# Kernel tuning notes

Measured on AMD Instinct MI355X. Metric: run time of the kernel, lower is better.

The kernel has to match this reference:

```python
import jax, jax.numpy as jnp
import numpy as np

T = 2048        # Tmax encoder frames
EPROJS = 1024   # encoder projection dim (Henc)
DUNITS = 512    # prediction net hidden
EMBED = 512     # embedding dim
JOINT = 512     # joint space dim
ODIM = 10000    # output vocab
BLANK = 0


def setup_inputs() -> dict:
    key = jax.random.key(0)
    ks = jax.random.split(key, 11)
    def g(k, shape, scale):
        return (jax.random.normal(k, shape, dtype=jnp.float32) * scale)
    inp = {
        'h': jax.random.normal(ks[0], (T, EPROJS), dtype=jnp.float32),
        # Embedding with padding_idx=blank -> blank row zeroed
        'embed': g(ks[1], (ODIM, EMBED), 0.05).at[BLANK].set(0.0),
        # LSTMCell params (torch gate order: i, f, g, o)
        'W_ih': g(ks[2], (4 * DUNITS, EMBED), 1.0 / np.sqrt(EMBED)),
        'W_hh': g(ks[3], (4 * DUNITS, DUNITS), 1.0 / np.sqrt(DUNITS)),
        'b_ih': g(ks[4], (4 * DUNITS,), 0.01),
        'b_hh': g(ks[5], (4 * DUNITS,), 0.01),
        # joint network
        'W_enc': g(ks[6], (JOINT, EPROJS), 1.0 / np.sqrt(EPROJS)),
        'b_enc': g(ks[7], (JOINT,), 0.01),
        'W_dec': g(ks[8], (JOINT, DUNITS), 1.0 / np.sqrt(DUNITS)),  # no bias
        'W_out': g(ks[9], (ODIM, JOINT), 1.0 / np.sqrt(JOINT)),
        'b_out': g(ks[10], (ODIM,), 0.01),
    }
    return inp


def _lstm_cell(x, h_prev, c_prev, W_ih, W_hh, b_ih, b_hh):
    gates = W_ih @ x + b_ih + W_hh @ h_prev + b_hh  # (4*DUNITS,)
    i, f, g, o = jnp.split(gates, 4)
    c = jax.nn.sigmoid(f) * c_prev + jax.nn.sigmoid(i) * jnp.tanh(g)
    h = jax.nn.sigmoid(o) * jnp.tanh(c)
    return h, c


def reference(h, embed, W_ih, W_hh, b_ih, b_hh, W_enc, b_enc, W_dec, W_out, b_out):
    # Precompute encoder-side joint projection (same math, hoisted out of loop)
    h_proj = h @ W_enc.T + b_enc  # (T, JOINT)

    # Initial prediction-net step on zero embedding from zero state
    zeros_e = jnp.zeros((EMBED,), dtype=h.dtype)
    zeros_d = jnp.zeros((DUNITS,), dtype=h.dtype)
    y0, c0 = _lstm_cell(zeros_e, zeros_d, zeros_d, W_ih, W_hh, b_ih, b_hh)

    def step(carry, hp_t):
        y, c, score = carry
        # joint: tanh(lin_enc(h_t) + lin_dec(y)) -> lin_out -> log_softmax
        ytu = jax.nn.log_softmax(W_out @ jnp.tanh(hp_t + W_dec @ y) + b_out)
        logp = jnp.max(ytu)
        pred = jnp.argmax(ytu)
        emitted = pred != BLANK
        # Candidate prediction-net update with embedded token
        ey = embed[pred]
        y_new, c_new = _lstm_cell(ey, y, c, W_ih, W_hh, b_ih, b_hh)
        y = jnp.where(emitted, y_new, y)
        c = jnp.where(emitted, c_new, c)
        score = score + jnp.where(emitted, logp, jnp.zeros_like(logp))
        tok = jnp.where(emitted, pred, BLANK).astype(jnp.int32)
        return (y, c, score), tok

    (y, c, score), yseq = jax.lax.scan(step, (y0, c0, jnp.float32(0.0)), h_proj)
    # yseq: (T,) int32, BLANK where no symbol was emitted at that frame
    return yseq, score
```

## Files before the change

### kernel.cpp

```cpp
#include <hip/hip_runtime.h>
#include <stdint.h>

typedef unsigned long long u64;
typedef uint32_t u32;

#define NB     256
#define NT     256
#define TMAX   2048
#define EPROJS 1024
#define DUNITS 512
#define EMBED  512
#define JOINT  512
#define ODIM   10000

#define N_LSTM 32
#define CONS0  32
#define N_CONS 223
#define AGG_B  255
#define MAGIC  0xD07ED07Eu

#define WS_PK   0
#define WS_SA   7168
#define WS_DN   14336
#define WS_AGG  15360
#define WS_Y    16384
#define WS_U    20480
#define WS_PART 24576
#define WS_HP   155648

__device__ __forceinline__ float aloadf(const float* p){
  return __hip_atomic_load(p, __ATOMIC_RELAXED, __HIP_MEMORY_SCOPE_AGENT);
}
__device__ __forceinline__ void astoref(float* p, float v){
  __hip_atomic_store(p, v, __ATOMIC_RELAXED, __HIP_MEMORY_SCOPE_AGENT);
}
__device__ __forceinline__ u64 aloadu64(const u64* p){
  return __hip_atomic_load(p, __ATOMIC_RELAXED, __HIP_MEMORY_SCOPE_AGENT);
}
__device__ __forceinline__ void astoreu64(u64* p, u64 v){
  __hip_atomic_store(p, v, __ATOMIC_RELAXED, __HIP_MEMORY_SCOPE_AGENT);
}
__device__ __forceinline__ u32 aloadu32(const u32* p){
  return __hip_atomic_load(p, __ATOMIC_RELAXED, __HIP_MEMORY_SCOPE_AGENT);
}
__device__ __forceinline__ void astoreu32(u32* p, u32 v){
  __hip_atomic_store(p, v, __ATOMIC_RELAXED, __HIP_MEMORY_SCOPE_AGENT);
}

__device__ __forceinline__ u32 ordbits(float f){
  u32 u = __float_as_uint(f);
  return (u & 0x80000000u) ? ~u : (u | 0x80000000u);
}
__device__ __forceinline__ float unordbits(u32 o){
  u32 u = (o & 0x80000000u) ? (o & 0x7fffffffu) : ~o;
  return __uint_as_float(u);
}
__device__ __forceinline__ float sigmoidf_(float x){ return 1.0f/(1.0f+expf(-x)); }

__device__ __forceinline__ float wredsum(float v){
  #pragma unroll
  for (int o=32;o>0;o>>=1) v += __shfl_xor(v, o);
  return v;
}
__device__ __forceinline__ u64 wredmax64(u64 v){
  #pragma unroll
  for (int o=32;o>0;o>>=1){ u64 x = __shfl_xor(v, o); v = (x>v)?x:v; }
  return v;
}

__device__ __forceinline__ int zslot(int j){
  return (j&7)*64 + ((j>>3) ^ ((j&7)<<2));
}

#define LOAD8(dst, baseptr) { const float4* _p=(const float4*)(baseptr); \
  float4 _a=_p[0], _b=_p[1]; \
  dst[0]=_a.x; dst[1]=_a.y; dst[2]=_a.z; dst[3]=_a.w; \
  dst[4]=_b.x; dst[5]=_b.y; dst[6]=_b.z; dst[7]=_b.w; }

__global__ void rnnt_init(char* ws){
  u32* p = (u32*)ws;
  const int stride = blockDim.x * gridDim.x;
  for (int i = blockIdx.x*blockDim.x + threadIdx.x; i < 38912; i += stride) p[i] = 0u;
}

__global__ void __launch_bounds__(NT, 1)
rnnt_decode(const float* __restrict__ h,    const float* __restrict__ embed,
            const float* __restrict__ W_ih, const float* __restrict__ W_hh,
            const float* __restrict__ b_ih, const float* __restrict__ b_hh,
            const float* __restrict__ W_enc,const float* __restrict__ b_enc,
            const float* __restrict__ W_dec,const float* __restrict__ W_out,
            const float* __restrict__ b_out,
            float* __restrict__ out, char* __restrict__ ws)
{
  const int b    = blockIdx.x;
  const int tid  = threadIdx.x;
  const int lane = tid & 63;
  const int w    = tid >> 6;

  u64*  ytag  = (u64*)(ws + WS_Y);
  u64*  utag  = (u64*)(ws + WS_U);
  u64*  ptag  = (u64*)(ws + WS_PART);
  u64*  pkall = (u64*)(ws + WS_PK);
  u64*  saall = (u64*)(ws + WS_SA);
  u32*  done  = (u32*)(ws + WS_DN);
  u32*  aggr  = (u32*)(ws + WS_AGG);
  float* hp   = (float*)(ws + WS_HP);

  __shared__ float smem[8192];
  float* PL = smem;
  float* GL = &smem[4416];
  u64*   R64= (u64*)&smem[4480];
  float* RF = &smem[4488];
  float* YO = &smem[4492];
  float* ZL = &smem[4544];
  float* PS = &smem[5056];

  {
    float (*lds_h)[EPROJS] = (float(*)[EPROJS])smem;
    #pragma unroll
    for (int r=0;r<8;r++){
      const float4 hv = *(const float4*)(h + (size_t)(8*b + r)*EPROJS + tid*4);
      *(float4*)&lds_h[r][tid*4] = hv;
    }
    __syncthreads();
    for (int p=0;p<2;p++){
      const int j = p*NT + tid;
      float acc[8] = {0,0,0,0,0,0,0,0};
      const float4* wrow = (const float4*)(W_enc + (size_t)j*EPROJS);
      for (int k4=0;k4<EPROJS/4;k4++){
        const float4 wv = wrow[k4];
        #pragma unroll
        for (int t8=0;t8<8;t8++){
          const float4 hv = *(const float4*)&lds_h[t8][k4*4];
          acc[t8] = fmaf(wv.x,hv.x, fmaf(wv.y,hv.y, fmaf(wv.z,hv.z, fmaf(wv.w,hv.w, acc[t8]))));
        }
      }
      const float be = b_enc[j];
      #pragma unroll
      for (int t8=0;t8<8;t8++)
        astoref(&hp[(size_t)(8*b+t8)*JOINT + j], acc[t8] + be);
    }
    asm volatile("s_waitcnt vmcnt(0)" ::: "memory");
    if (tid==0) astoreu32(&done[b], MAGIC);
    __syncthreads();
  }

  if (b < N_LSTM){
    const int d = b;
    float wih[16][8], whh[16][8];
    #pragma unroll
    for (int q=0;q<16;q++){
      const int gr = w*DUNITS + 16*d + q;
      LOAD8(wih[q], W_ih + (size_t)gr*EMBED  + lane*8);
      LOAD8(whh[q], W_hh + (size_t)gr*DUNITS + lane*8);
    }
    float wdc0[16], wdc1[16];
    {
      const float4* p0 = (const float4*)(W_dec + (size_t)(2*tid)*DUNITS   + 16*d);
      const float4* p1 = (const float4*)(W_dec + (size_t)(2*tid+1)*DUNITS + 16*d);
      #pragma unroll
      for (int k4=0;k4<4;k4++){
        const float4 a = p0[k4];
        wdc0[4*k4+0]=a.x; wdc0[4*k4+1]=a.y; wdc0[4*k4+2]=a.z; wdc0[4*k4+3]=a.w;
        const float4 c = p1[k4];
        wdc1[4*k4+0]=c.x; wdc1[4*k4+1]=c.y; wdc1[4*k4+2]=c.z; wdc1[4*k4+3]=c.w;
      }
    }
    float bias_r = 0.0f;
    if (tid < 64){
      const int gr = (tid>>4)*DUNITS + 16*d + (tid&15);
      bias_r = b_ih[gr] + b_hh[gr];
    }
    float c_st = 0.0f, y_st = 0.0f;
    if (tid < 16){
      const int j = 16*d + tid;
      const float gi = b_ih[j]            + b_hh[j];
      const float gg = b_ih[2*DUNITS + j] + b_hh[2*DUNITS + j];
      const float go = b_ih[3*DUNITS + j] + b_hh[3*DUNITS + j];
      c_st = sigmoidf_(gi)*tanhf(gg);
      y_st = sigmoidf_(go)*tanhf(c_st);
      YO[tid] = y_st;
      astoreu64(&ytag[j], ((u64)1u<<32) | (u64)__float_as_uint(y_st));
    }
    __syncthreads();
    {
      float p0=0.f, p1=0.f;
      #pragma unroll
      for (int k=0;k<16;k++){ p0 = fmaf(wdc0[k], YO[k], p0); p1 = fmaf(wdc1[k], YO[k], p1); }
      u64* up = ptag + (size_t)d*512;
      astoreu64(&up[2*tid],   ((u64)1u<<32) | (u64)__float_as_uint(p0));
      astoreu64(&up[2*tid+1], ((u64)1u<<32) | (u64)__float_as_uint(p1));
    }

    const int jj = tid & 15;
    const int pp = tid >> 4;
    for (int t=0;t<TMAX;t++){
      const u32 g = (u32)(t+1);
      u64 pv0, pv1, yv[8];
      for(;;){
        pv0 = aloadu64(&ptag[(size_t)(2*pp)*512   + 16*d + jj]);
        pv1 = aloadu64(&ptag[(size_t)(2*pp+1)*512 + 16*d + jj]);
        bool ok = ((u32)(pv0>>32)==g) & ((u32)(pv1>>32)==g);
        #pragma unroll
        for (int i=0;i<8;i++){
          yv[i] = aloadu64(&ytag[8*lane + i]);
          ok &= ((u32)(yv[i]>>32) == g);
        }
        if (ok) break;
        __builtin_amdgcn_s_sleep(1);
      }
      float y8[8];
      #pragma unroll
      for (int i=0;i<8;i++) y8[i] = __uint_as_float((u32)yv[i]);
      PS[jj*17 + pp] = __uint_as_float((u32)pv0) + __uint_as_float((u32)pv1);
      __syncthreads();
      if (tid < 16){
        float s = 0.f;
        #pragma unroll
        for (int k=0;k<16;k++) s += PS[tid*17 + k];
        astoreu64(&utag[16*d + tid], ((u64)g<<32) | (u64)__float_as_uint(s));
      }
      float vp[16];
      #pragma unroll
      for (int q=0;q<16;q++){
        float a=0.f;
        #pragma unroll
        for (int k=0;k<8;k++) a = fmaf(whh[q][k], y8[k], a);
        vp[q] = a;
      }
      u64 pk = 0;
      {
        const u64* pks = pkall + (g&3)*224;
        for(;;){
          pk = (tid < N_CONS) ? aloadu64(&pks[tid]) : 0;
          const int ok = (tid < N_CONS) ? ((u32)(pk>>48) >= g) : 1;
          if (__all(ok)) break;
          __builtin_amdgcn_s_sleep(1);
        }
      }
      const u64 m = wredmax64(pk);
      if (lane==0) R64[w] = m;
      const int predw = (int)((~(u32)m) & 0xFFFFu);
      float e8[8];
      LOAD8(e8, embed + (size_t)predw*EMBED + 8*lane);
      __syncthreads();
      u64 best = R64[0];
      #pragma unroll
      for (int i=1;i<4;i++){ const u64 x=R64[i]; best = (x>best)?x:best; }
      const int pred = (int)((~(u32)best) & 0xFFFFu);
      const int emitted = (pred != 0);
      if (m != best){
        LOAD8(e8, embed + (size_t)pred*EMBED + 8*lane);
      }
      #pragma unroll
      for (int q=0;q<16;q++){
        float a = vp[q];
        #pragma unroll
        for (int k=0;k<8;k++) a = fmaf(wih[q][k], e8[k], a);
        PL[(w*16+q)*68 + lane] = a;
      }
      __syncthreads();
      if (tid < 64){
        const float* row = &PL[tid*68];
        float s = bias_r;
        #pragma unroll
        for (int k4=0;k4<16;k4++){
          const float4 v4 = *(const float4*)&row[4*k4];
          s += v4.x + v4.y + v4.z + v4.w;
        }
        GL[tid] = s;
      }
      __syncthreads();
      if (tid < 16){
        const float gi=GL[tid], gf=GL[16+tid], gg=GL[32+tid], go=GL[48+tid];
        const float cn = sigmoidf_(gf)*c_st + sigmoidf_(gi)*tanhf(gg);
        const float yn = sigmoidf_(go)*tanhf(cn);
        if (emitted){ c_st = cn; y_st = yn; }
        YO[tid] = y_st;
        if (t < TMAX-1)
          astoreu64(&ytag[16*d + tid], ((u64)(g+1)<<32) | (u64)__float_as_uint(y_st));
      }
      __syncthreads();
      if (t < TMAX-1){
        float p0=0.f, p1=0.f;
        #pragma unroll
        for (int k=0;k<16;k++){ p0 = fmaf(wdc0[k], YO[k], p0); p1 = fmaf(wdc1[k], YO[k], p1); }
        u64* up = ptag + (size_t)d*512;
        astoreu64(&up[2*tid],   ((u64)(g+1)<<32) | (u64)__float_as_uint(p0));
        astoreu64(&up[2*tid+1], ((u64)(g+1)<<32) | (u64)__float_as_uint(p1));
      }
    }
  }
  else if (b < AGG_B){
    const int cb = b - CONS0;
    int rowstart, rowcnt;
    if (cb < 188){ rowstart = cb*45;                 rowcnt = 45; }
    else         { rowstart = 8460 + (cb-188)*44;    rowcnt = 44; }
    float wout[12][8];
    #pragma unroll
    for (int q=0;q<12;q++){
      const int s = 12*w + q;
      if (s < rowcnt){
        LOAD8(wout[q], W_out + (size_t)(rowstart+s)*JOINT + lane*8);
      } else {
        #pragma unroll
        for (int k=0;k<8;k++) wout[q][k]=0.f;
      }
    }
    float my_bo = 0.f; int my_row = 0; bool my_val = false;
    if (tid < rowcnt){ my_val = true; my_row = rowstart + tid; my_bo = b_out[my_row]; }
    const u32* agrep = &aggr[(cb&7)*32];

    for(;;){
      const u32 dv = aloadu32(&done[tid]);
      if (__all(dv == MAGIC)) break;
      __builtin_amdgcn_s_sleep(2);
    }
    __syncthreads();

    const int j0 = 2*tid, j1 = 2*tid+1;
    const int s0 = zslot(j0), s1 = zslot(j1);
    for (int t=0;t<TMAX;t++){
      const u32 g = (u32)(t+1);
      const float2 h2 = *(const float2*)(hp + (size_t)t*JOINT + j0);
      u64 ua, ub2;
      for(;;){
        ua  = aloadu64(&utag[j0]);
        ub2 = aloadu64(&utag[j1]);
        if ( (((u32)(ua>>32))==g) & (((u32)(ub2>>32))==g) ) break;
        __builtin_amdgcn_s_sleep(1);
      }
      ZL[s0] = tanhf(h2.x + __uint_as_float((u32)ua));
      ZL[s1] = tanhf(h2.y + __uint_as_float((u32)ub2));
      __syncthreads();
      float z8[8];
      #pragma unroll
      for (int e=0;e<8;e++) z8[e] = ZL[e*64 + (lane ^ (e<<2))];
      #pragma unroll
      for (int q=0;q<12;q++){
        float a=0.f;
        #pragma unroll
        for (int k=0;k<8;k++) a = fmaf(wout[q][k], z8[k], a);
        PL[(12*w+q)*68 + lane] = a;
      }
      __syncthreads();
      u64 key = 0; float lg = 0.f;
      if (tid < 48){
        const float* row = &PL[tid*68];
        float s = my_bo;
        #pragma unroll
        for (int k4=0;k4<16;k4++){
          const float4 v4 = *(const float4*)&row[4*k4];
          s += v4.x + v4.y + v4.z + v4.w;
        }
        lg = s;
        if (my_val) key = ((u64)ordbits(lg)<<16) | (u64)(0xFFFFu & ~(u32)my_row);
      }
      if (w == 0){
        const u64 bk = wredmax64(key);
        const float mw = unordbits((u32)(bk>>16));
        const float e  = my_val ? __expf(lg - mw) : 0.f;
        const float sw = wredsum(e);
        if (lane == 0){
          while ((int)(g - aloadu32(agrep)) > 3) __builtin_amdgcn_s_sleep(2);
          astoreu64(&saall[(g&3)*224 + cb], ((u64)g<<32) | (u64)__float_as_uint(sw));
          astoreu64(&pkall[(g&3)*224 + cb], ((u64)g<<48) | bk);
        }
      }
    }
  }
  else {
    float score = 0.0f;
    for (int t=0;t<TMAX;t++){
      const u32 g = (u32)(t+1);
      const u64* pks = pkall + (g&3)*224;
      const u64* sas = saall + (g&3)*224;
      u64 pk=0, sa=0;
      for(;;){
        if (tid < N_CONS){ pk = aloadu64(&pks[tid]); sa = aloadu64(&sas[tid]); }
        const int ok = (tid < N_CONS) ? (((u32)(pk>>48)==g) & (((u32)(sa>>32))==g)) : 1;
        if (__all(ok)) break;
        __builtin_amdgcn_s_sleep(2);
      }
      { u64 m = wredmax64(pk); if (lane==0) R64[w]=m; }
      __syncthreads();
      u64 best = R64[0];
      #pragma unroll
      for (int i=1;i<4;i++){ const u64 x=R64[i]; best = (x>best)?x:best; }
      const float mstar = unordbits((u32)(best>>16));
      float term = (tid < N_CONS) ?
        __uint_as_float((u32)sa) * __expf(unordbits((u32)(pk>>16)) - mstar) : 0.f;
      term = wredsum(term);
      if (lane==0) RF[w] = term;
      __syncthreads();
      if (tid==0){
        const float S = RF[0]+RF[1]+RF[2]+RF[3];
        const int pred = (int)((~(u32)best) & 0xFFFFu);
        if (pred != 0) score += -logf(S);
        out[t] = (float)pred;
      }
      __syncthreads();
      if (tid < 8) astoreu32(&aggr[tid*32], g);
    }
    if (tid==0) out[TMAX] = score;
  }
}

extern "C" void kernel_launch(void* const* d_in, const int* in_sizes, int n_in,
                              void* d_out, int out_size, void* d_ws, size_t ws_size,
                              hipStream_t stream)
{
  const float* h     = (const float*)d_in[0];
  const float* embed = (const float*)d_in[1];
  const float* W_ih  = (const float*)d_in[2];
  const float* W_hh  = (const float*)d_in[3];
  const float* b_ih  = (const float*)d_in[4];
  const float* b_hh  = (const float*)d_in[5];
  const float* W_enc = (const float*)d_in[6];
  const float* b_enc = (const float*)d_in[7];
  const float* W_dec = (const float*)d_in[8];
  const float* W_out = (const float*)d_in[9];
  const float* b_out = (const float*)d_in[10];
  float* out = (float*)d_out;
  char* ws = (char*)d_ws;

  hipLaunchKernelGGL(rnnt_init, dim3(32), dim3(NT), 0, stream, ws);
  hipLaunchKernelGGL(rnnt_decode, dim3(NB), dim3(NT), 0, stream,
                     h, embed, W_ih, W_hh, b_ih, b_hh, W_enc, b_enc, W_dec, W_out, b_out,
                     out, ws);
}
```

Before: 17.70 ms.

## Replace tagged partial-sum exchange with atomicAdd reduction and counter barrier

LSTM blocks now accumulate their W_dec partial products straight into a double-buffered, 8-way replicated float buffer with atomicAdd and bump per-replica counters. Consumer blocks spin on a single counter and sum the 8 replicas themselves. This removes the second-level tagged reduction stage in the LSTM blocks and the per-element tag polling, and swaps wave-level __all spins with sleeps for block-wide __syncthreads_and polling. The cost is float atomics (non-deterministic summation order), explicit zeroing of buffers each step, and extra block barriers.

```diff
diff --git a/kernel.cpp b/kernel.cpp
--- a/kernel.cpp
+++ b/kernel.cpp
@@ -23,10 +23,10 @@
 #define WS_SA   7168
 #define WS_DN   14336
 #define WS_AGG  15360
-#define WS_Y    16384
-#define WS_U    20480
-#define WS_PART 24576
-#define WS_HP   155648
+#define WS_CNT  16384
+#define WS_Y    17408
+#define WS_U    21504
+#define WS_HP   54272
 
 __device__ __forceinline__ float aloadf(const float* p){
   return __hip_atomic_load(p, __ATOMIC_RELAXED, __HIP_MEMORY_SCOPE_AGENT);
@@ -80,7 +80,7 @@
 __global__ void rnnt_init(char* ws){
   u32* p = (u32*)ws;
   const int stride = blockDim.x * gridDim.x;
-  for (int i = blockIdx.x*blockDim.x + threadIdx.x; i < 38912; i += stride) p[i] = 0u;
+  for (int i = blockIdx.x*blockDim.x + threadIdx.x; i < 13568; i += stride) p[i] = 0u;
 }
 
 __global__ void __launch_bounds__(NT, 1)
@@ -97,13 +97,13 @@
   const int lane = tid & 63;
   const int w    = tid >> 6;
 
-  u64*  ytag  = (u64*)(ws + WS_Y);
-  u64*  utag  = (u64*)(ws + WS_U);
-  u64*  ptag  = (u64*)(ws + WS_PART);
+  u64*   ytag = (u64*)(ws + WS_Y);
+  float* ubuf = (float*)(ws + WS_U);
   u64*  pkall = (u64*)(ws + WS_PK);
   u64*  saall = (u64*)(ws + WS_SA);
   u32*  done  = (u32*)(ws + WS_DN);
   u32*  aggr  = (u32*)(ws + WS_AGG);
+  u32*  cnt   = (u32*)(ws + WS_CNT);
   float* hp   = (float*)(ws + WS_HP);
 
   __shared__ float smem[8192];
@@ -112,8 +112,7 @@
   u64*   R64= (u64*)&smem[4480];
   float* RF = &smem[4488];
   float* YO = &smem[4492];
-  float* ZL = &smem[4544];
-  float* PS = &smem[5056];
+  float* SL = &smem[4544];
 
   {
     float (*lds_h)[EPROJS] = (float(*)[EPROJS])smem;
@@ -187,39 +186,28 @@
       float p0=0.f, p1=0.f;
       #pragma unroll
       for (int k=0;k<16;k++){ p0 = fmaf(wdc0[k], YO[k], p0); p1 = fmaf(wdc1[k], YO[k], p1); }
-      u64* up = ptag + (size_t)d*512;
-      astoreu64(&up[2*tid],   ((u64)1u<<32) | (u64)__float_as_uint(p0));
-      astoreu64(&up[2*tid+1], ((u64)1u<<32) | (u64)__float_as_uint(p1));
-    }
-
-    const int jj = tid & 15;
-    const int pp = tid >> 4;
+      float* up = ubuf + 1*4096 + (d&7)*512;
+      atomicAdd(&up[2*tid],   p0);
+      atomicAdd(&up[2*tid+1], p1);
+    }
+    asm volatile("s_waitcnt vmcnt(0)" ::: "memory");
+    __syncthreads();
+    if (tid < 8) atomicAdd(&cnt[tid*32], 1u);
+
     for (int t=0;t<TMAX;t++){
       const u32 g = (u32)(t+1);
-      u64 pv0, pv1, yv[8];
+      u64 ya, yb;
       for(;;){
-        pv0 = aloadu64(&ptag[(size_t)(2*pp)*512   + 16*d + jj]);
-        pv1 = aloadu64(&ptag[(size_t)(2*pp+1)*512 + 16*d + jj]);
-        bool ok = ((u32)(pv0>>32)==g) & ((u32)(pv1>>32)==g);
-        #pragma unroll
-        for (int i=0;i<8;i++){
-          yv[i] = aloadu64(&ytag[8*lane + i]);
-          ok &= ((u32)(yv[i]>>32) == g);
-        }
-        if (ok) break;
-        __builtin_amdgcn_s_sleep(1);
-      }
+        ya = aloadu64(&ytag[2*tid]); yb = aloadu64(&ytag[2*tid+1]);
+        const int ok = ((u32)(ya>>32)==g) & ((u32)(yb>>32)==g);
+        if (__syncthreads_and(ok)) break;
+      }
+      SL[zslot(2*tid)]   = __uint_as_float((u32)ya);
+      SL[zslot(2*tid+1)] = __uint_as_float((u32)yb);
+      __syncthreads();
       float y8[8];
       #pragma unroll
-      for (int i=0;i<8;i++) y8[i] = __uint_as_float((u32)yv[i]);
-      PS[jj*17 + pp] = __uint_as_float((u32)pv0) + __uint_as_float((u32)pv1);
-      __syncthreads();
-      if (tid < 16){
-        float s = 0.f;
-        #pragma unroll
-        for (int k=0;k<16;k++) s += PS[tid*17 + k];
-        astoreu64(&utag[16*d + tid], ((u64)g<<32) | (u64)__float_as_uint(s));
-      }
+      for (int e=0;e<8;e++) y8[e] = SL[e*64 + (lane ^ (e<<2))];
       float vp[16];
       #pragma unroll
       for (int q=0;q<16;q++){
@@ -229,14 +217,10 @@
         vp[q] = a;
       }
       u64 pk = 0;
-      {
-        const u64* pks = pkall + (g&3)*224;
-        for(;;){
-          pk = (tid < N_CONS) ? aloadu64(&pks[tid]) : 0;
-          const int ok = (tid < N_CONS) ? ((u32)(pk>>48) >= g) : 1;
-          if (__all(ok)) break;
-          __builtin_amdgcn_s_sleep(1);
-        }
+      for(;;){
+        if (tid < N_CONS) pk = aloadu64(&pkall[(g&3)*224 + tid]);
+        const int ok = (tid < N_CONS) ? ((u32)(pk>>48) >= g) : 1;
+        if (__syncthreads_and(ok)) break;
       }
       const u64 m = wredmax64(pk);
       if (lane==0) R64[w] = m;
@@ -251,6 +235,10 @@
       const int emitted = (pred != 0);
       if (m != best){
         LOAD8(e8, embed + (size_t)pred*EMBED + 8*lane);
+      }
+      if (tid < 64){
+        u64* uz = (u64*)(ubuf + (g&1)*4096 + (d&7)*512) + (d>>3)*64;
+        astoreu64(&uz[tid], 0ull);
       }
       #pragma unroll
       for (int q=0;q<16;q++){
@@ -285,10 +273,13 @@
         float p0=0.f, p1=0.f;
         #pragma unroll
         for (int k=0;k<16;k++){ p0 = fmaf(wdc0[k], YO[k], p0); p1 = fmaf(wdc1[k], YO[k], p1); }
-        u64* up = ptag + (size_t)d*512;
-        astoreu64(&up[2*tid],   ((u64)(g+1)<<32) | (u64)__float_as_uint(p0));
-        astoreu64(&up[2*tid+1], ((u64)(g+1)<<32) | (u64)__float_as_uint(p1));
-      }
+        float* up = ubuf + ((g+1)&1)*4096 + (d&7)*512;
+        atomicAdd(&up[2*tid],   p0);
+        atomicAdd(&up[2*tid+1], p1);
+      }
+      asm volatile("s_waitcnt vmcnt(0)" ::: "memory");
+      __syncthreads();
+      if (t < TMAX-1 && tid < 8) atomicAdd(&cnt[tid*32], 1u);
     }
   }
   else if (b < AGG_B){
@@ -312,30 +303,36 @@
     const u32* agrep = &aggr[(cb&7)*32];
 
     for(;;){
-      const u32 dv = aloadu32(&done[tid]);
-      if (__all(dv == MAGIC)) break;
-      __builtin_amdgcn_s_sleep(2);
-    }
-    __syncthreads();
-
+      const int ok = (aloadu32(&done[tid]) == MAGIC);
+      if (__syncthreads_and(ok)) break;
+    }
+
+    const u32* cp = &cnt[(cb&7)*32];
     const int j0 = 2*tid, j1 = 2*tid+1;
     const int s0 = zslot(j0), s1 = zslot(j1);
     for (int t=0;t<TMAX;t++){
       const u32 g = (u32)(t+1);
       const float2 h2 = *(const float2*)(hp + (size_t)t*JOINT + j0);
-      u64 ua, ub2;
-      for(;;){
-        ua  = aloadu64(&utag[j0]);
-        ub2 = aloadu64(&utag[j1]);
-        if ( (((u32)(ua>>32))==g) & (((u32)(ub2>>32))==g) ) break;
-        __builtin_amdgcn_s_sleep(1);
-      }
-      ZL[s0] = tanhf(h2.x + __uint_as_float((u32)ua));
-      ZL[s1] = tanhf(h2.y + __uint_as_float((u32)ub2));
+      if (tid==0){ while (aloadu32(cp) < 32u*g) {} }
+      __syncthreads();
+      float u0 = 0.f, u1 = 0.f;
+      {
+        const u64* ub64 = (const u64*)(ubuf + (g&1)*4096) + tid;
+        u64 v[8];
+        #pragma unroll
+        for (int r=0;r<8;r++) v[r] = aloadu64(ub64 + r*256);
+        #pragma unroll
+        for (int r=0;r<8;r++){
+          u0 += __uint_as_float((u32)v[r]);
+          u1 += __uint_as_float((u32)(v[r]>>32));
+        }
+      }
+      SL[s0] = tanhf(h2.x + u0);
+      SL[s1] = tanhf(h2.y + u1);
       __syncthreads();
       float z8[8];
       #pragma unroll
-      for (int e=0;e<8;e++) z8[e] = ZL[e*64 + (lane ^ (e<<2))];
+      for (int e=0;e<8;e++) z8[e] = SL[e*64 + (lane ^ (e<<2))];
       #pragma unroll
       for (int q=0;q<12;q++){
         float a=0.f;
@@ -367,6 +364,7 @@
           astoreu64(&pkall[(g&3)*224 + cb], ((u64)g<<48) | bk);
         }
       }
+      __syncthreads();
     }
   }
   else {
@@ -379,8 +377,7 @@
       for(;;){
         if (tid < N_CONS){ pk = aloadu64(&pks[tid]); sa = aloadu64(&sas[tid]); }
         const int ok = (tid < N_CONS) ? (((u32)(pk>>48)==g) & (((u32)(sa>>32))==g)) : 1;
-        if (__all(ok)) break;
-        __builtin_amdgcn_s_sleep(2);
+        if (__syncthreads_and(ok)) break;
       }
       { u64 m = wredmax64(pk); if (lane==0) R64[w]=m; }
       __syncthreads();
```

Result: faster. 16.71 ms (-5.6%).
